# Kernel tuning notes

Hardware: AMD Instinct MI355X
Metric: run time of the kernel (lower is better)

The kernel has to match this reference:

```python
import jax, jax.numpy as jnp
import numpy as np

S = 4096
T_STEPS = 2048

def setup_inputs() -> dict:
    key = jax.random.key(0)
    k1, k2, k3 = jax.random.split(key, 3)
    # initial log-prior over S states
    log_M0 = jax.nn.log_softmax(jax.random.normal(k1, (S,), dtype=jnp.float32))
    # transition log-probs: log_trans[i, j] = log p(x_t = i | x_{t-1} = j)
    # (logsumexp in the torch code is over dim=1 = previous state, so columns normalize)
    log_trans = jax.nn.log_softmax(jax.random.normal(k2, (S, S), dtype=jnp.float32), axis=0)
    # per-step emission log-likelihoods log f_t(y_t | x_t), t = 0..T
    log_emit = 0.5 * jax.random.normal(k3, (T_STEPS + 1, S), dtype=jnp.float32)
    return {"log_M0": log_M0, "log_trans": log_trans, "log_emit": log_emit, "T": T_STEPS}

def reference(log_M0, log_trans, log_emit, T):
    # initialise(): unnormalized filter at t=0
    unnorm0 = log_M0 + log_emit[0]                       # [S]
    lf0 = jax.nn.logsumexp(unnorm0)                      # scalar log-normalizer
    filt0 = unnorm0 - lf0

    def step(carry, emit_t):
        filt, lik = carry
        # prediction_i = logsumexp_j( filter_j + log_trans[i, j] )
        pred = jax.nn.logsumexp(filt[None, :] + log_trans, axis=1)   # [S]
        unnorm = pred + emit_t                                        # [S]
        lf = jax.nn.logsumexp(unnorm)
        return (unnorm - lf, lik + lf), None

    (_, likelihood), _ = jax.lax.scan(step, (filt0, lf0), log_emit[1:T + 1])
    # forward() returns the accumulated sum of per-step likelihood factors = total log-likelihood
    return likelihood
```

## Files before the change

### kernel.cpp

```cpp
#include <hip/hip_runtime.h>

#define SS 4096
#define TT 2048

typedef float v4f __attribute__((ext_vector_type(4)));
typedef unsigned u2 __attribute__((ext_vector_type(2)));


__device__ __forceinline__ void llc_load4x4(const v4f* p,
                                            v4f& a, v4f& b, v4f& c, v4f& d) {
  asm volatile(
      "global_load_dwordx4 %0, %4, off sc0 sc1\n\t"
      "global_load_dwordx4 %1, %5, off sc0 sc1\n\t"
      "global_load_dwordx4 %2, %6, off sc0 sc1\n\t"
      "global_load_dwordx4 %3, %7, off sc0 sc1\n\t"
      "s_waitcnt vmcnt(0)"
      : "=&v"(a), "=&v"(b), "=&v"(c), "=&v"(d)
      : "v"(p), "v"(p + 256), "v"(p + 512), "v"(p + 768)
      : "memory");
}

__device__ __forceinline__ void llc_sent4(const float* p0, const float* p1,
                                          const float* p2, const float* p3,
                                          float& a, float& b, float& c, float& d) {
  asm volatile(
      "global_load_dword %0, %4, off sc0 sc1\n\t"
      "global_load_dword %1, %5, off sc0 sc1\n\t"
      "global_load_dword %2, %6, off sc0 sc1\n\t"
      "global_load_dword %3, %7, off sc0 sc1\n\t"
      "s_waitcnt vmcnt(0)"
      : "=&v"(a), "=&v"(b), "=&v"(c), "=&v"(d)
      : "v"(p0), "v"(p1), "v"(p2), "v"(p3)
      : "memory");
}

__device__ __forceinline__ void llc_store4_drain(v4f* p, v4f v) {
  asm volatile("global_store_dwordx4 %0, %1, off sc0 sc1\n\t"
               "s_waitcnt vmcnt(0)"
               :: "v"(p), "v"(v) : "memory");
}


__device__ __forceinline__ unsigned short f2bf_rn(float f) {
  unsigned int u = __float_as_uint(f);
  u += 0x7FFFu + ((u >> 16) & 1u);
  return (unsigned short)(u >> 16);
}

__device__ __forceinline__ unsigned pkbf(float a, float b) {
  return (unsigned)f2bf_rn(a) | ((unsigned)f2bf_rn(b) << 16);
}

__device__ __forceinline__ float blo(unsigned w) { return __uint_as_float(w << 16); }
__device__ __forceinline__ float bhi(unsigned w) { return __uint_as_float(w & 0xFFFF0000u); }

__device__ __forceinline__ v4f fma4(u2 e, v4f q, v4f a) {
  a.x = fmaf(blo(e.x), q.x, a.x);
  a.y = fmaf(bhi(e.x), q.y, a.y);
  a.z = fmaf(blo(e.y), q.z, a.z);
  a.w = fmaf(bhi(e.y), q.w, a.w);
  return a;
}

__device__ __forceinline__ unsigned orsgn(v4f v, unsigned e) {
  return (__float_as_uint(v.x) ^ e) | (__float_as_uint(v.y) ^ e)
       | (__float_as_uint(v.z) ^ e) | (__float_as_uint(v.w) ^ e);
}

__global__ void init_q(const float* __restrict__ m0, const float* __restrict__ emit,
                       float* __restrict__ q) {
  int i = blockIdx.x * 256 + threadIdx.x;
  q[i] = __expf(m0[i] + emit[i]);
}

#define K16(X) X(0) X(1) X(2) X(3) X(4) X(5) X(6) X(7) \
               X(8) X(9) X(10) X(11) X(12) X(13) X(14) X(15)

__global__ void __launch_bounds__(256, 1) __attribute__((amdgpu_waves_per_eu(1, 1)))
hmm_fwd(const float* __restrict__ lt, const float* __restrict__ emit,
        float* q, float* out) {
  __shared__ float qs[2][SS];
  __shared__ float wsum[4];
  const int b    = blockIdx.x;
  const int tid  = threadIdx.x;
  const int wave = tid >> 6;
  const int lane = tid & 63;
  const int row0 = (b << 4) + (wave << 2);

#define DECL_E(k) u2 e0_##k, e1_##k, e2_##k, e3_##k;
  K16(DECL_E)
#undef DECL_E

  {
    const float* s0 = lt + (size_t)row0 * SS + (lane << 2);
    const float* s1 = s0 + SS;
    const float* s2 = s1 + SS;
    const float* s3 = s2 + SS;
#define INIT_E(k) { \
    v4f t0 = *(const v4f*)(s0 + ((k) << 8)); \
    v4f t1 = *(const v4f*)(s1 + ((k) << 8)); \
    v4f t2 = *(const v4f*)(s2 + ((k) << 8)); \
    v4f t3 = *(const v4f*)(s3 + ((k) << 8)); \
    e0_##k = (u2){pkbf(__expf(t0.x), __expf(t0.y)), pkbf(__expf(t0.z), __expf(t0.w))}; \
    e1_##k = (u2){pkbf(__expf(t1.x), __expf(t1.y)), pkbf(__expf(t1.z), __expf(t1.w))}; \
    e2_##k = (u2){pkbf(__expf(t2.x), __expf(t2.y)), pkbf(__expf(t2.z), __expf(t2.w))}; \
    e3_##k = (u2){pkbf(__expf(t3.x), __expf(t3.y)), pkbf(__expf(t3.z), __expf(t3.w))}; }
    K16(INIT_E)
#undef INIT_E
  }

  for (int t = 1; t <= TT; ++t) {
    v4f em;
    if (lane == 0) em = *(const v4f*)(emit + (size_t)t * SS + row0);

    const unsigned e = (unsigned)(((t - 1) >> 1) & 1) << 31;
    {
      const v4f* qsrc4 = (const v4f*)(q + ((t - 1) & 1) * SS);
      v4f va, vb, vc, vd;
      llc_load4x4(qsrc4 + tid, va, vb, vc, vd);
      unsigned o = orsgn(va, e) | orsgn(vb, e) | orsgn(vc, e) | orsgn(vd, e);
      if (o >> 31) {
        const float* qw = (const float*)qsrc4;
        const float* p0 = qw + (tid << 2);
        const float* p1 = p0 + 1024;
        const float* p2 = p0 + 2048;
        const float* p3 = p0 + 3072;
        for (;;) {
          float s0v, s1v, s2v, s3v;
          llc_sent4(p0, p1, p2, p3, s0v, s1v, s2v, s3v);
          unsigned so = (__float_as_uint(s0v) ^ e) | (__float_as_uint(s1v) ^ e)
                      | (__float_as_uint(s2v) ^ e) | (__float_as_uint(s3v) ^ e);
          if (!(so >> 31)) break;
        }
        llc_load4x4(qsrc4 + tid, va, vb, vc, vd);
      }
      v4f* qsb = (v4f*)qs[t & 1];
      qsb[tid]       = va;
      qsb[tid + 256] = vb;
      qsb[tid + 512] = vc;
      qsb[tid + 768] = vd;
    }
    __syncthreads();

    v4f a0 = {0.f, 0.f, 0.f, 0.f}, a1 = a0, a2 = a0, a3 = a0;
    const v4f* qv4 = (const v4f*)qs[t & 1];
#define FMA_K(k) { \
    v4f qv = qv4[((k) << 6) + lane]; \
    a0 = fma4(e0_##k, qv, a0);  a1 = fma4(e1_##k, qv, a1); \
    a2 = fma4(e2_##k, qv, a2);  a3 = fma4(e3_##k, qv, a3); }
    K16(FMA_K)
#undef FMA_K

    float acc0 = (a0.x + a0.y) + (a0.z + a0.w);
    float acc1 = (a1.x + a1.y) + (a1.z + a1.w);
    float acc2 = (a2.x + a2.y) + (a2.z + a2.w);
    float acc3 = (a3.x + a3.y) + (a3.z + a3.w);
#pragma unroll
    for (int m = 32; m > 0; m >>= 1) {
      acc0 += __shfl_xor(acc0, m);
      acc1 += __shfl_xor(acc1, m);
      acc2 += __shfl_xor(acc2, m);
      acc3 += __shfl_xor(acc3, m);
    }

    if (lane == 0) {
      float scale = ((t & 255) == 0) ? 0x1p-46f : 1.0f;
      if (!(t & 1)) scale = -scale;
      v4f r;
      r.x = acc0 * (__expf(em.x) * scale);
      r.y = acc1 * (__expf(em.y) * scale);
      r.z = acc2 * (__expf(em.z) * scale);
      r.w = acc3 * (__expf(em.w) * scale);
      llc_store4_drain((v4f*)(q + (t & 1) * SS + row0), r);
    }
  }

  if (b == 0) {
    const v4f* qf4 = (const v4f*)q;
    v4f va, vb, vc, vd;
    for (;;) {
      llc_load4x4(qf4 + tid, va, vb, vc, vd);
      unsigned o = orsgn(va, 0) | orsgn(vb, 0) | orsgn(vc, 0) | orsgn(vd, 0);
      if (!(o >> 31)) break;
    }
    float s = va.x + va.y + va.z + va.w + vb.x + vb.y + vb.z + vb.w
            + vc.x + vc.y + vc.z + vc.w + vd.x + vd.y + vd.z + vd.w;
#pragma unroll
    for (int m = 32; m > 0; m >>= 1) s += __shfl_xor(s, m);
    if (lane == 0) wsum[wave] = s;
    __syncthreads();
    if (tid == 0) {
      float tot = wsum[0] + wsum[1] + wsum[2] + wsum[3];
      out[0] = logf(tot) + 368.0f * 0.693147180559945f;
    }
  }
}

extern "C" void kernel_launch(void* const* d_in, const int* in_sizes, int n_in,
                              void* d_out, int out_size, void* d_ws, size_t ws_size,
                              hipStream_t stream) {
  const float* log_M0    = (const float*)d_in[0];
  const float* log_trans = (const float*)d_in[1];
  const float* log_emit  = (const float*)d_in[2];

  float* q   = (float*)d_ws;
  float* out = (float*)d_out;

  hipLaunchKernelGGL(init_q, dim3(SS / 256), dim3(256), 0, stream, log_M0, log_emit, q);
  hipLaunchKernelGGL(hmm_fwd, dim3(256), dim3(256), 0, stream, log_trans, log_emit, q, out);
}
```

Baseline: 5.090 ms.

## Drop store drain, forward own rows via LDS, prefetch emissions

Each block's step-output store no longer waits on vmcnt. The block's own freshly computed rows are kept in LDS and substituted into the next step's vector, and the poll loop ignores sign checks for those rows, so a block never waits on the global visibility of its own writes. The next step's emission values are prefetched, and their exp is computed before the barrier, taking a global load off the critical path. In exchange, a second workgroup barrier is added per step, plus an inline-asm register keep-alive so the in-flight store's source registers are not reused too early.

New measurement: 8.792 ms. +72.7%, slower.

```diff
diff --git a/kernel.cpp b/kernel.cpp
--- a/kernel.cpp
+++ b/kernel.cpp
@@ -34,10 +34,13 @@
       : "memory");
 }
 
-__device__ __forceinline__ void llc_store4_drain(v4f* p, v4f v) {
-  asm volatile("global_store_dwordx4 %0, %1, off sc0 sc1\n\t"
-               "s_waitcnt vmcnt(0)"
-               :: "v"(p), "v"(v) : "memory");
+#define LLC_STORE4_NODRAIN(p, v) \
+  asm volatile("global_store_dwordx4 %0, %1, off sc0 sc1" \
+               :: "v"(p), "v"(v) : "memory")
+
+__device__ __forceinline__ void bar_lgkm() {
+  asm volatile("s_waitcnt lgkmcnt(0)" ::: "memory");
+  __builtin_amdgcn_s_barrier();
 }
 
 
@@ -80,12 +83,17 @@
 hmm_fwd(const float* __restrict__ lt, const float* __restrict__ emit,
         float* q, float* out) {
   __shared__ float qs[2][SS];
+  __shared__ v4f qown[4];
   __shared__ float wsum[4];
   const int b    = blockIdx.x;
   const int tid  = threadIdx.x;
   const int wave = tid >> 6;
   const int lane = tid & 63;
   const int row0 = (b << 4) + (wave << 2);
+
+  const int  ownth  = tid - ((b & 63) << 2);
+  const bool is_own = ((unsigned)ownth) < 4u;
+  const int  ownq   = b >> 6;
 
 #define DECL_E(k) u2 e0_##k, e1_##k, e2_##k, e3_##k;
   K16(DECL_E)
@@ -109,17 +117,28 @@
 #undef INIT_E
   }
 
+  if (lane == 0) qown[wave] = *(const v4f*)(q + row0);
+  v4f em;
+  if (lane == 0) em = *(const v4f*)(emit + (size_t)1 * SS + row0);
+  v4f r_keep = {0.f, 0.f, 0.f, 0.f};
+  __syncthreads();
+
   for (int t = 1; t <= TT; ++t) {
-    v4f em;
-    if (lane == 0) em = *(const v4f*)(emit + (size_t)t * SS + row0);
-
     const unsigned e = (unsigned)(((t - 1) >> 1) & 1) << 31;
+    const v4f* qsrc4 = (const v4f*)(q + ((t - 1) & 1) * SS);
+    v4f va, vb, vc, vd;
+    llc_load4x4(qsrc4 + tid, va, vb, vc, vd);
+    asm volatile("" :: "v"(r_keep));
     {
-      const v4f* qsrc4 = (const v4f*)(q + ((t - 1) & 1) * SS);
-      v4f va, vb, vc, vd;
-      llc_load4x4(qsrc4 + tid, va, vb, vc, vd);
-      unsigned o = orsgn(va, e) | orsgn(vb, e) | orsgn(vc, e) | orsgn(vd, e);
-      if (o >> 31) {
+      unsigned o0 = orsgn(va, e), o1 = orsgn(vb, e),
+               o2 = orsgn(vc, e), o3 = orsgn(vd, e);
+      if (is_own) {
+        if      (ownq == 0) o0 = 0;
+        else if (ownq == 1) o1 = 0;
+        else if (ownq == 2) o2 = 0;
+        else                o3 = 0;
+      }
+      if ((o0 | o1 | o2 | o3) >> 31) {
         const float* qw = (const float*)qsrc4;
         const float* p0 = qw + (tid << 2);
         const float* p1 = p0 + 1024;
@@ -128,19 +147,40 @@
         for (;;) {
           float s0v, s1v, s2v, s3v;
           llc_sent4(p0, p1, p2, p3, s0v, s1v, s2v, s3v);
-          unsigned so = (__float_as_uint(s0v) ^ e) | (__float_as_uint(s1v) ^ e)
-                      | (__float_as_uint(s2v) ^ e) | (__float_as_uint(s3v) ^ e);
-          if (!(so >> 31)) break;
+          unsigned w0 = __float_as_uint(s0v) ^ e, w1 = __float_as_uint(s1v) ^ e,
+                   w2 = __float_as_uint(s2v) ^ e, w3 = __float_as_uint(s3v) ^ e;
+          if (is_own) {
+            if      (ownq == 0) w0 = 0;
+            else if (ownq == 1) w1 = 0;
+            else if (ownq == 2) w2 = 0;
+            else                w3 = 0;
+          }
+          if (!((w0 | w1 | w2 | w3) >> 31)) break;
         }
         llc_load4x4(qsrc4 + tid, va, vb, vc, vd);
       }
+    }
+    if (is_own) {
+      v4f ov = qown[ownth];
+      if      (ownq == 0) va = ov;
+      else if (ownq == 1) vb = ov;
+      else if (ownq == 2) vc = ov;
+      else                vd = ov;
+    }
+    {
       v4f* qsb = (v4f*)qs[t & 1];
       qsb[tid]       = va;
       qsb[tid + 256] = vb;
       qsb[tid + 512] = vc;
       qsb[tid + 768] = vd;
     }
-    __syncthreads();
+    v4f ex;
+    if (lane == 0) {
+      ex.x = __expf(em.x);  ex.y = __expf(em.y);
+      ex.z = __expf(em.z);  ex.w = __expf(em.w);
+      if (t < TT) em = *(const v4f*)(emit + (size_t)(t + 1) * SS + row0);
+    }
+    bar_lgkm();
 
     v4f a0 = {0.f, 0.f, 0.f, 0.f}, a1 = a0, a2 = a0, a3 = a0;
     const v4f* qv4 = (const v4f*)qs[t & 1];
@@ -167,13 +207,19 @@
       float scale = ((t & 255) == 0) ? 0x1p-46f : 1.0f;
       if (!(t & 1)) scale = -scale;
       v4f r;
-      r.x = acc0 * (__expf(em.x) * scale);
-      r.y = acc1 * (__expf(em.y) * scale);
-      r.z = acc2 * (__expf(em.z) * scale);
-      r.w = acc3 * (__expf(em.w) * scale);
-      llc_store4_drain((v4f*)(q + (t & 1) * SS + row0), r);
-    }
+      r.x = acc0 * (ex.x * scale);
+      r.y = acc1 * (ex.y * scale);
+      r.z = acc2 * (ex.z * scale);
+      r.w = acc3 * (ex.w * scale);
+      LLC_STORE4_NODRAIN((v4f*)(q + (t & 1) * SS + row0), r);
+      qown[wave] = r;
+      r_keep = r;
+    }
+    bar_lgkm();
   }
+
+  asm volatile("" :: "v"(r_keep));
+  asm volatile("s_waitcnt vmcnt(0)" ::: "memory");
 
   if (b == 0) {
     const v4f* qf4 = (const v4f*)q;
```

## Split rows across 8 waves per block and add backoff in spin poll

Applied to the files above, without the earlier changes.

Doubles the block to 512 threads, so each wave owns 2 rows instead of 4. This halves the per-wave register-resident bf16 transition slice and the FMA and shuffle work per step. The per-step q gather and LDS fill are split across more threads, and the sentinel poll gains a dummy LDS read as a short delay. The intent is to shorten the serial critical path of each time step. In exchange it adds more waves contending at the barrier and more stores per step.

After: 4.722 ms. -7.2%, faster.

```diff
diff --git a/kernel.cpp b/kernel.cpp
--- a/kernel.cpp
+++ b/kernel.cpp
@@ -4,8 +4,19 @@
 #define TT 2048
 
 typedef float v4f __attribute__((ext_vector_type(4)));
+typedef float v2f __attribute__((ext_vector_type(2)));
 typedef unsigned u2 __attribute__((ext_vector_type(2)));
 
+
+__device__ __forceinline__ void llc_load2(const v4f* p, v4f& a, v4f& b) {
+  asm volatile(
+      "global_load_dwordx4 %0, %2, off sc0 sc1\n\t"
+      "global_load_dwordx4 %1, %3, off sc0 sc1\n\t"
+      "s_waitcnt vmcnt(0)"
+      : "=&v"(a), "=&v"(b)
+      : "v"(p), "v"(p + 512)
+      : "memory");
+}
 
 __device__ __forceinline__ void llc_load4x4(const v4f* p,
                                             v4f& a, v4f& b, v4f& c, v4f& d) {
@@ -34,10 +45,18 @@
       : "memory");
 }
 
-__device__ __forceinline__ void llc_store4_drain(v4f* p, v4f v) {
-  asm volatile("global_store_dwordx4 %0, %1, off sc0 sc1\n\t"
+__device__ __forceinline__ void llc_store2_drain(float* p, v2f v) {
+  asm volatile("global_store_dwordx2 %0, %1, off sc0 sc1\n\t"
                "s_waitcnt vmcnt(0)"
                :: "v"(p), "v"(v) : "memory");
+}
+
+__device__ __forceinline__ void straggle_tick(int lane) {
+  float dummy;
+  asm volatile("ds_read_b32 %0, %1\n\t"
+               "s_waitcnt lgkmcnt(0)"
+               : "=v"(dummy) : "v"(lane << 7) : "memory");
+  asm volatile("" :: "v"(dummy));
 }
 
 
@@ -76,7 +95,7 @@
 #define K16(X) X(0) X(1) X(2) X(3) X(4) X(5) X(6) X(7) \
                X(8) X(9) X(10) X(11) X(12) X(13) X(14) X(15)
 
-__global__ void __launch_bounds__(256, 1) __attribute__((amdgpu_waves_per_eu(1, 1)))
+__global__ void __launch_bounds__(512, 1) __attribute__((amdgpu_waves_per_eu(2, 2)))
 hmm_fwd(const float* __restrict__ lt, const float* __restrict__ emit,
         float* q, float* out) {
   __shared__ float qs[2][SS];
@@ -85,109 +104,98 @@
   const int tid  = threadIdx.x;
   const int wave = tid >> 6;
   const int lane = tid & 63;
-  const int row0 = (b << 4) + (wave << 2);
-
-#define DECL_E(k) u2 e0_##k, e1_##k, e2_##k, e3_##k;
+  const int row0 = (b << 4) + (wave << 1);
+
+#define DECL_E(k) u2 e0_##k, e1_##k;
   K16(DECL_E)
 #undef DECL_E
 
   {
     const float* s0 = lt + (size_t)row0 * SS + (lane << 2);
     const float* s1 = s0 + SS;
-    const float* s2 = s1 + SS;
-    const float* s3 = s2 + SS;
 #define INIT_E(k) { \
     v4f t0 = *(const v4f*)(s0 + ((k) << 8)); \
     v4f t1 = *(const v4f*)(s1 + ((k) << 8)); \
-    v4f t2 = *(const v4f*)(s2 + ((k) << 8)); \
-    v4f t3 = *(const v4f*)(s3 + ((k) << 8)); \
     e0_##k = (u2){pkbf(__expf(t0.x), __expf(t0.y)), pkbf(__expf(t0.z), __expf(t0.w))}; \
-    e1_##k = (u2){pkbf(__expf(t1.x), __expf(t1.y)), pkbf(__expf(t1.z), __expf(t1.w))}; \
-    e2_##k = (u2){pkbf(__expf(t2.x), __expf(t2.y)), pkbf(__expf(t2.z), __expf(t2.w))}; \
-    e3_##k = (u2){pkbf(__expf(t3.x), __expf(t3.y)), pkbf(__expf(t3.z), __expf(t3.w))}; }
+    e1_##k = (u2){pkbf(__expf(t1.x), __expf(t1.y)), pkbf(__expf(t1.z), __expf(t1.w))}; }
     K16(INIT_E)
 #undef INIT_E
   }
 
   for (int t = 1; t <= TT; ++t) {
-    v4f em;
-    if (lane == 0) em = *(const v4f*)(emit + (size_t)t * SS + row0);
+    v2f em;
+    if (lane == 0) em = *(const v2f*)(emit + (size_t)t * SS + row0);
 
     const unsigned e = (unsigned)(((t - 1) >> 1) & 1) << 31;
     {
       const v4f* qsrc4 = (const v4f*)(q + ((t - 1) & 1) * SS);
-      v4f va, vb, vc, vd;
-      llc_load4x4(qsrc4 + tid, va, vb, vc, vd);
-      unsigned o = orsgn(va, e) | orsgn(vb, e) | orsgn(vc, e) | orsgn(vd, e);
+      v4f va, vb;
+      llc_load2(qsrc4 + tid, va, vb);
+      unsigned o = orsgn(va, e) | orsgn(vb, e);
       if (o >> 31) {
         const float* qw = (const float*)qsrc4;
         const float* p0 = qw + (tid << 2);
-        const float* p1 = p0 + 1024;
+        const float* p1 = p0 + 2;
         const float* p2 = p0 + 2048;
-        const float* p3 = p0 + 3072;
+        const float* p3 = p0 + 2050;
         for (;;) {
+          straggle_tick(lane);
           float s0v, s1v, s2v, s3v;
           llc_sent4(p0, p1, p2, p3, s0v, s1v, s2v, s3v);
           unsigned so = (__float_as_uint(s0v) ^ e) | (__float_as_uint(s1v) ^ e)
                       | (__float_as_uint(s2v) ^ e) | (__float_as_uint(s3v) ^ e);
           if (!(so >> 31)) break;
         }
-        llc_load4x4(qsrc4 + tid, va, vb, vc, vd);
+        llc_load2(qsrc4 + tid, va, vb);
       }
       v4f* qsb = (v4f*)qs[t & 1];
       qsb[tid]       = va;
-      qsb[tid + 256] = vb;
-      qsb[tid + 512] = vc;
-      qsb[tid + 768] = vd;
+      qsb[tid + 512] = vb;
     }
     __syncthreads();
 
-    v4f a0 = {0.f, 0.f, 0.f, 0.f}, a1 = a0, a2 = a0, a3 = a0;
+    v4f a0 = {0.f, 0.f, 0.f, 0.f}, a1 = a0;
     const v4f* qv4 = (const v4f*)qs[t & 1];
 #define FMA_K(k) { \
     v4f qv = qv4[((k) << 6) + lane]; \
-    a0 = fma4(e0_##k, qv, a0);  a1 = fma4(e1_##k, qv, a1); \
-    a2 = fma4(e2_##k, qv, a2);  a3 = fma4(e3_##k, qv, a3); }
+    a0 = fma4(e0_##k, qv, a0);  a1 = fma4(e1_##k, qv, a1); }
     K16(FMA_K)
 #undef FMA_K
 
     float acc0 = (a0.x + a0.y) + (a0.z + a0.w);
     float acc1 = (a1.x + a1.y) + (a1.z + a1.w);
-    float acc2 = (a2.x + a2.y) + (a2.z + a2.w);
-    float acc3 = (a3.x + a3.y) + (a3.z + a3.w);
 #pragma unroll
     for (int m = 32; m > 0; m >>= 1) {
       acc0 += __shfl_xor(acc0, m);
       acc1 += __shfl_xor(acc1, m);
-      acc2 += __shfl_xor(acc2, m);
-      acc3 += __shfl_xor(acc3, m);
     }
 
     if (lane == 0) {
       float scale = ((t & 255) == 0) ? 0x1p-46f : 1.0f;
       if (!(t & 1)) scale = -scale;
-      v4f r;
+      v2f r;
       r.x = acc0 * (__expf(em.x) * scale);
       r.y = acc1 * (__expf(em.y) * scale);
-      r.z = acc2 * (__expf(em.z) * scale);
-      r.w = acc3 * (__expf(em.w) * scale);
-      llc_store4_drain((v4f*)(q + (t & 1) * SS + row0), r);
+      llc_store2_drain(q + (t & 1) * SS + row0, r);
     }
   }
 
   if (b == 0) {
-    const v4f* qf4 = (const v4f*)q;
-    v4f va, vb, vc, vd;
-    for (;;) {
-      llc_load4x4(qf4 + tid, va, vb, vc, vd);
-      unsigned o = orsgn(va, 0) | orsgn(vb, 0) | orsgn(vc, 0) | orsgn(vd, 0);
-      if (!(o >> 31)) break;
-    }
-    float s = va.x + va.y + va.z + va.w + vb.x + vb.y + vb.z + vb.w
-            + vc.x + vc.y + vc.z + vc.w + vd.x + vd.y + vd.z + vd.w;
+    float s = 0.f;
+    if (tid < 256) {
+      const v4f* qf4 = (const v4f*)q;
+      v4f va, vb, vc, vd;
+      for (;;) {
+        llc_load4x4(qf4 + tid, va, vb, vc, vd);
+        unsigned o = orsgn(va, 0) | orsgn(vb, 0) | orsgn(vc, 0) | orsgn(vd, 0);
+        if (!(o >> 31)) break;
+      }
+      s = va.x + va.y + va.z + va.w + vb.x + vb.y + vb.z + vb.w
+        + vc.x + vc.y + vc.z + vc.w + vd.x + vd.y + vd.z + vd.w;
 #pragma unroll
-    for (int m = 32; m > 0; m >>= 1) s += __shfl_xor(s, m);
-    if (lane == 0) wsum[wave] = s;
+      for (int m = 32; m > 0; m >>= 1) s += __shfl_xor(s, m);
+      if (lane == 0) wsum[wave] = s;
+    }
     __syncthreads();
     if (tid == 0) {
       float tot = wsum[0] + wsum[1] + wsum[2] + wsum[3];
@@ -207,5 +215,5 @@
   float* out = (float*)d_out;
 
   hipLaunchKernelGGL(init_q, dim3(SS / 256), dim3(256), 0, stream, log_M0, log_emit, q);
-  hipLaunchKernelGGL(hmm_fwd, dim3(256), dim3(256), 0, stream, log_trans, log_emit, q, out);
-}
+  hipLaunchKernelGGL(hmm_fwd, dim3(256), dim3(512), 0, stream, log_trans, log_emit, q, out);
+}
```
